# Performance work log

Measured on AMD Instinct MI355X. Metric: run time of the kernel, lower is better.

## Reference

```python
import jax, jax.numpy as jnp
import numpy as np

B, S, QD, DM, H = 8, 4096, 4, 1024, 16
HD = DM // H
NROT = 4
EPS_LN = 1e-5


def layer_norm(x, g, b):
    m = x.mean(axis=-1, keepdims=True)
    v = ((x - m) ** 2).mean(axis=-1, keepdims=True)
    return (x - m) / jnp.sqrt(v + EPS_LN) * g + b


def quat_normalize(q):
    return q / (jnp.linalg.norm(q, axis=-1, keepdims=True) + 1e-8)


def quat_multiply(a, b):
    w1, x1, y1, z1 = a[..., 0], a[..., 1], a[..., 2], a[..., 3]
    w2, x2, y2, z2 = b[..., 0], b[..., 1], b[..., 2], b[..., 3]
    return jnp.stack([
        w1 * w2 - x1 * x2 - y1 * y2 - z1 * z2,
        w1 * x2 + x1 * w2 + y1 * z2 - z1 * y2,
        w1 * y2 - x1 * z2 + y1 * w2 + z1 * x2,
        w1 * z2 + x1 * y2 - y1 * x2 + z1 * w2,
    ], axis=-1)


def quat_conjugate(q):
    return q * jnp.array([1.0, -1.0, -1.0, -1.0], dtype=q.dtype)


def unit_quaternion(theta):  # theta: [3]
    c0, c1, c2 = jnp.cos(theta[0] / 2), jnp.cos(theta[1] / 2), jnp.cos(theta[2] / 2)
    s0, s1, s2 = jnp.sin(theta[0] / 2), jnp.sin(theta[1] / 2), jnp.sin(theta[2] / 2)
    q = jnp.stack([c0 * c1 * c2, s0 * c1 * c2, c0 * s1 * c2, c0 * c1 * s2])
    return quat_normalize(q)


def fractal_alpha(x):  # x: [B, S, DM] -> alpha: [B]
    xf = x.reshape(x.shape[0], -1)
    ps = jnp.abs(jnp.fft.rfft(xf, axis=-1)) ** 2  # [B, N/2+1]
    freqs = jnp.fft.rfftfreq(xf.shape[-1]).astype(x.dtype)
    w = ((freqs > 0.01) & (freqs < 0.5)).astype(x.dtype)
    n = w.sum()
    log_k = jnp.log(freqs + 1e-10)
    log_P = jnp.log(ps + 1e-10)
    mk = (w * log_k).sum() / n
    mP = (w * log_P).sum(axis=-1) / n  # [B]
    dk = (log_k - mk)
    cov = (w * dk * (log_P - mP[:, None])).sum(axis=-1)
    var = (w * dk * dk).sum()
    beta = -cov / (var + 1e-10)
    D = jnp.clip((3.0 - beta) / 2.0, 0.5, 1.5)
    # alpha(D) = alpha_base*(1 + lambda*(D - D_e)/D_e), base=1.0, lambda=0.8, D_e=1.0
    return jnp.clip(1.0 * (1.0 + 0.8 * (D - 1.0)), 0.1, 3.0)


def spectral_attention(x, alpha_base, phase_shift, W_attn_out, b_attn_out, ln_g, ln_b):
    # x: [B, S, DM]
    alpha = jax.lax.stop_gradient(fractal_alpha(x))  # [B]  (torch.no_grad)
    xh = x.reshape(B, S, H, HD).transpose(0, 2, 1, 3)  # [B, H, S, HD]
    x_fft = jnp.fft.fft(xh, axis=2)  # complex [B, H, S, HD]
    freqs = jnp.fft.fftfreq(S).astype(x.dtype)  # [S]
    log_k = jnp.log(jnp.abs(freqs) + 1e-8)
    log_kn = (log_k - log_k.mean()) / (jnp.std(log_k, ddof=1) + 1e-8)
    gelu_k = jax.nn.gelu(log_kn, approximate=False)  # [S]
    # phase[b,h,s] = alpha_base[h]*alpha[b]*gelu_k[s] + phase_shift[h]
    phase = (alpha_base[None, :, None] * alpha[:, None, None] * gelu_k[None, None, :]
             + phase_shift[None, :, None])  # [B, H, S]
    kernel = jnp.exp(1j * phase.astype(jnp.float32))[..., None]  # [B, H, S, 1]
    x_filt = jnp.fft.ifft(x_fft * kernel, axis=2).real  # [B, H, S, HD]
    out = x_filt.transpose(0, 2, 1, 3).reshape(B, S, DM)
    out = out @ W_attn_out + b_attn_out  # out_proj; dropout = identity (eval)
    return layer_norm(x + out, ln_g, ln_b)


def so4_evolution(q, theta_L, theta_R):  # q: [B, S, 4]
    out = q
    for i in range(NROT):
        qL = unit_quaternion(theta_L[i])
        qR_conj = quat_conjugate(unit_quaternion(theta_R[i]))
        out = quat_multiply(quat_multiply(jnp.broadcast_to(qL, out.shape), out),
                            jnp.broadcast_to(qR_conj, out.shape))
        out = quat_normalize(out)
    return out


def setup_inputs() -> dict:
    key = jax.random.key(0)
    ks = jax.random.split(key, 24)
    def rn(k, shape, scale=0.02):
        return jax.random.normal(k, shape, dtype=jnp.float32) * scale
    return {
        "x": jax.random.normal(ks[0], (B, S, QD), dtype=jnp.float32),
        "W_in": rn(ks[1], (QD, DM)), "b_in": jnp.zeros((DM,), jnp.float32),
        "alpha_base": jnp.ones((H,), jnp.float32),
        "phase_shift": jnp.zeros((H,), jnp.float32),
        "W_attn_out": rn(ks[2], (DM, DM)), "b_attn_out": jnp.zeros((DM,), jnp.float32),
        "ln_attn_g": jnp.ones((DM,), jnp.float32), "ln_attn_b": jnp.zeros((DM,), jnp.float32),
        "W_out": rn(ks[3], (DM, QD)), "b_out": jnp.zeros((QD,), jnp.float32),
        "theta_L": rn(ks[4], (NROT, 3), 0.1), "theta_R": rn(ks[5], (NROT, 3), 0.1),
        "W_ff1": rn(ks[6], (QD, 4 * QD)), "b_ff1": jnp.zeros((4 * QD,), jnp.float32),
        "W_ff2": rn(ks[7], (4 * QD, QD)), "b_ff2": jnp.zeros((QD,), jnp.float32),
        "n1_g": jnp.ones((QD,), jnp.float32), "n1_b": jnp.zeros((QD,), jnp.float32),
        "n2_g": jnp.ones((QD,), jnp.float32), "n2_b": jnp.zeros((QD,), jnp.float32),
        "n3_g": jnp.ones((QD,), jnp.float32), "n3_b": jnp.zeros((QD,), jnp.float32),
    }


def reference(x, W_in, b_in, alpha_base, phase_shift, W_attn_out, b_attn_out,
              ln_attn_g, ln_attn_b, W_out, b_out, theta_L, theta_R,
              W_ff1, b_ff1, W_ff2, b_ff2, n1_g, n1_b, n2_g, n2_b, n3_g, n3_b):
    x_proj = x @ W_in + b_in  # [B, S, DM]
    attn = spectral_attention(x_proj, alpha_base, phase_shift, W_attn_out, b_attn_out,
                              ln_attn_g, ln_attn_b)
    attn_quat = attn @ W_out + b_out  # [B, S, 4]
    h = quat_normalize(layer_norm(x + attn_quat, n1_g, n1_b))
    evolved = so4_evolution(h, theta_L, theta_R)
    h = quat_normalize(layer_norm(h + evolved, n2_g, n2_b))
    ff = jax.nn.gelu(h @ W_ff1 + b_ff1, approximate=False) @ W_ff2 + b_ff2
    h = quat_normalize(layer_norm(h + ff, n3_g, n3_b))
    return h
```

## Files before the change

### kernel.cpp

```cpp
#include <hip/hip_runtime.h>
#include <hip/hip_bf16.h>
#include <math.h>


#define DEV static __device__ __forceinline__
typedef unsigned int uint32;
typedef unsigned short u16;

typedef __attribute__((ext_vector_type(8))) _Float16 f16x8;
typedef __attribute__((ext_vector_type(4))) float f32x4;
typedef __attribute__((ext_vector_type(2))) unsigned int u32x2;

DEV float2 cmulf(float2 a, float2 b) {
  return make_float2(a.x * b.x - a.y * b.y, a.x * b.y + a.y * b.x);
}
DEV u16 f2h(float f) {
  union { _Float16 h; u16 u; } v;
  v.h = (_Float16)f;
  return v.u;
}
DEV float h2f(uint32 u) {
  union { u16 s; _Float16 h; } v;
  v.s = (u16)u;
  return (float)v.h;
}
DEV uint32 pack2h(float a, float b) {
  return (uint32)f2h(a) | ((uint32)f2h(b) << 16);
}
DEV void glds16(void* lds, const void* g) {
  __builtin_amdgcn_global_load_lds((const __attribute__((address_space(1))) unsigned int*)g,
                                   (__attribute__((address_space(3))) unsigned int*)lds, 16, 0, 0);
}
DEV void wave_sync() {
  asm volatile("s_waitcnt lgkmcnt(0)" ::: "memory");
  __builtin_amdgcn_sched_barrier(0);
}
DEV int dr10(int v) {
  int r = (int)(__brev((unsigned)v) >> 22);
  return ((r & 0x155) << 1) | ((r & 0x2AA) >> 1);
}
constexpr int dr6c(int v) {
  return ((v & 3) << 4) | (v & 12) | ((v >> 4) & 3);
}

constexpr float CQ[17] = {
  1.0f, 0.995184726672197f, 0.980785280403230f, 0.956940335732209f,
  0.923879532511287f, 0.881921264348355f, 0.831469612302545f, 0.773010453362737f,
  0.707106781186548f, 0.634393284163645f, 0.555570233019602f, 0.471396736825998f,
  0.382683432365090f, 0.290284677254462f, 0.195090322016128f, 0.098017140329561f, 0.0f };
constexpr float twc64(int j) {
  return (j & 63) <= 16 ? CQ[j & 63]
       : (j & 63) <= 32 ? -CQ[32 - (j & 63)]
       : (j & 63) <= 48 ? -CQ[(j & 63) - 32] : CQ[64 - (j & 63)];
}
constexpr float tws64(int j) {
  return (j & 63) <= 16 ? CQ[16 - (j & 63)]
       : (j & 63) <= 32 ? CQ[(j & 63) - 16]
       : (j & 63) <= 48 ? -CQ[48 - (j & 63)] : -CQ[(j & 63) - 48];
}

constexpr float CR_C[16] = {
  1.0f, 0.980785280403230f, 0.923879532511287f, 0.831469612302545f,
  0.707106781186548f, 0.555570233019602f, 0.382683432365090f, 0.195090322016128f,
  0.0f, -0.195090322016128f, -0.382683432365090f, -0.555570233019602f,
  -0.707106781186548f, -0.831469612302545f, -0.923879532511287f, -0.980785280403230f };
constexpr float CR_S[16] = {
  0.0f, 0.195090322016128f, 0.382683432365090f, 0.555570233019602f,
  0.707106781186548f, 0.831469612302545f, 0.923879532511287f, 0.980785280403230f,
  1.0f, 0.980785280403230f, 0.923879532511287f, 0.831469612302545f,
  0.707106781186548f, 0.555570233019602f, 0.382683432365090f, 0.195090322016128f };

template<int SGN>
DEV void rdif64(float2* z) {
  #pragma unroll
  for (int j = 0; j < 16; ++j) {
    float2 x0 = z[j], x1 = z[j + 16], x2 = z[j + 32], x3 = z[j + 48];
    float2 s0 = make_float2(x0.x + x2.x, x0.y + x2.y);
    float2 s1 = make_float2(x0.x - x2.x, x0.y - x2.y);
    float2 s2 = make_float2(x1.x + x3.x, x1.y + x3.y);
    float2 d  = make_float2(x1.x - x3.x, x1.y - x3.y);
    float2 s3 = (SGN < 0) ? make_float2(d.y, -d.x) : make_float2(-d.y, d.x);
    z[j] = make_float2(s0.x + s2.x, s0.y + s2.y);
    const float2 tf1 = make_float2(twc64(j),     (float)SGN * tws64(j));
    const float2 tf2 = make_float2(twc64(2 * j), (float)SGN * tws64(2 * j));
    const float2 tf3 = make_float2(twc64(3 * j), (float)SGN * tws64(3 * j));
    z[j + 16] = cmulf(make_float2(s1.x + s3.x, s1.y + s3.y), tf1);
    z[j + 32] = cmulf(make_float2(s0.x - s2.x, s0.y - s2.y), tf2);
    z[j + 48] = cmulf(make_float2(s1.x - s3.x, s1.y - s3.y), tf3);
  }
  #pragma unroll
  for (int b = 0; b < 64; b += 16)
    #pragma unroll
    for (int j = 0; j < 4; ++j) {
      const int i = b + j;
      float2 x0 = z[i], x1 = z[i + 4], x2 = z[i + 8], x3 = z[i + 12];
      float2 s0 = make_float2(x0.x + x2.x, x0.y + x2.y);
      float2 s1 = make_float2(x0.x - x2.x, x0.y - x2.y);
      float2 s2 = make_float2(x1.x + x3.x, x1.y + x3.y);
      float2 d  = make_float2(x1.x - x3.x, x1.y - x3.y);
      float2 s3 = (SGN < 0) ? make_float2(d.y, -d.x) : make_float2(-d.y, d.x);
      z[i] = make_float2(s0.x + s2.x, s0.y + s2.y);
      const float2 tf1 = make_float2(twc64(4 * j),  (float)SGN * tws64(4 * j));
      const float2 tf2 = make_float2(twc64(8 * j),  (float)SGN * tws64(8 * j));
      const float2 tf3 = make_float2(twc64(12 * j), (float)SGN * tws64(12 * j));
      z[i + 4]  = cmulf(make_float2(s1.x + s3.x, s1.y + s3.y), tf1);
      z[i + 8]  = cmulf(make_float2(s0.x - s2.x, s0.y - s2.y), tf2);
      z[i + 12] = cmulf(make_float2(s1.x - s3.x, s1.y - s3.y), tf3);
    }
  #pragma unroll
  for (int b = 0; b < 64; b += 4) {
    float2 x0 = z[b], x1 = z[b + 1], x2 = z[b + 2], x3 = z[b + 3];
    float2 s0 = make_float2(x0.x + x2.x, x0.y + x2.y);
    float2 s1 = make_float2(x0.x - x2.x, x0.y - x2.y);
    float2 s2 = make_float2(x1.x + x3.x, x1.y + x3.y);
    float2 d  = make_float2(x1.x - x3.x, x1.y - x3.y);
    float2 s3 = (SGN < 0) ? make_float2(d.y, -d.x) : make_float2(-d.y, d.x);
    z[b]     = make_float2(s0.x + s2.x, s0.y + s2.y);
    z[b + 1] = make_float2(s1.x + s3.x, s1.y + s3.y);
    z[b + 2] = make_float2(s0.x - s2.x, s0.y - s2.y);
    z[b + 3] = make_float2(s1.x - s3.x, s1.y - s3.y);
  }
}

template<int SGN>
DEV void rdit64(float2* z) {
  #pragma unroll
  for (int b = 0; b < 64; b += 4) {
    float2 b0 = z[b], b1 = z[b + 1], b2 = z[b + 2], b3 = z[b + 3];
    float2 t0 = make_float2(b0.x + b2.x, b0.y + b2.y);
    float2 t1 = make_float2(b0.x - b2.x, b0.y - b2.y);
    float2 t2 = make_float2(b1.x + b3.x, b1.y + b3.y);
    float2 d  = make_float2(b1.x - b3.x, b1.y - b3.y);
    float2 t3 = (SGN > 0) ? make_float2(-d.y, d.x) : make_float2(d.y, -d.x);
    z[b]     = make_float2(t0.x + t2.x, t0.y + t2.y);
    z[b + 1] = make_float2(t1.x + t3.x, t1.y + t3.y);
    z[b + 2] = make_float2(t0.x - t2.x, t0.y - t2.y);
    z[b + 3] = make_float2(t1.x - t3.x, t1.y - t3.y);
  }
  #pragma unroll
  for (int b = 0; b < 64; b += 16)
    #pragma unroll
    for (int j = 0; j < 4; ++j) {
      const int i = b + j;
      const float2 tf1 = make_float2(twc64(4 * j),  (float)SGN * tws64(4 * j));
      const float2 tf2 = make_float2(twc64(8 * j),  (float)SGN * tws64(8 * j));
      const float2 tf3 = make_float2(twc64(12 * j), (float)SGN * tws64(12 * j));
      float2 b0 = z[i];
      float2 b1 = cmulf(z[i + 4], tf1);
      float2 b2 = cmulf(z[i + 8], tf2);
      float2 b3 = cmulf(z[i + 12], tf3);
      float2 t0 = make_float2(b0.x + b2.x, b0.y + b2.y);
      float2 t1 = make_float2(b0.x - b2.x, b0.y - b2.y);
      float2 t2 = make_float2(b1.x + b3.x, b1.y + b3.y);
      float2 d  = make_float2(b1.x - b3.x, b1.y - b3.y);
      float2 t3 = (SGN > 0) ? make_float2(-d.y, d.x) : make_float2(d.y, -d.x);
      z[i]      = make_float2(t0.x + t2.x, t0.y + t2.y);
      z[i + 4]  = make_float2(t1.x + t3.x, t1.y + t3.y);
      z[i + 8]  = make_float2(t0.x - t2.x, t0.y - t2.y);
      z[i + 12] = make_float2(t1.x - t3.x, t1.y - t3.y);
    }
  #pragma unroll
  for (int j = 0; j < 16; ++j) {
    const float2 tf1 = make_float2(twc64(j),     (float)SGN * tws64(j));
    const float2 tf2 = make_float2(twc64(2 * j), (float)SGN * tws64(2 * j));
    const float2 tf3 = make_float2(twc64(3 * j), (float)SGN * tws64(3 * j));
    float2 b0 = z[j];
    float2 b1 = cmulf(z[j + 16], tf1);
    float2 b2 = cmulf(z[j + 32], tf2);
    float2 b3 = cmulf(z[j + 48], tf3);
    float2 t0 = make_float2(b0.x + b2.x, b0.y + b2.y);
    float2 t1 = make_float2(b0.x - b2.x, b0.y - b2.y);
    float2 t2 = make_float2(b1.x + b3.x, b1.y + b3.y);
    float2 d  = make_float2(b1.x - b3.x, b1.y - b3.y);
    float2 t3 = (SGN > 0) ? make_float2(-d.y, d.x) : make_float2(d.y, -d.x);
    z[j]      = make_float2(t0.x + t2.x, t0.y + t2.y);
    z[j + 16] = make_float2(t1.x + t3.x, t1.y + t3.y);
    z[j + 32] = make_float2(t0.x - t2.x, t0.y - t2.y);
    z[j + 48] = make_float2(t1.x - t3.x, t1.y - t3.y);
  }
}

template<int L, int NLOG, int NSUB, bool WL>
DEV void dif4_stages(float2* F, int lg) {
  #pragma unroll
  for (int st = 0; st < NLOG / 2; ++st) {
    const int qlog = NLOG - 2 - 2 * st;
    const int q = 1 << qlog;
    float bs, bc;
    __sincosf((float)(lg & (q - 1)) * (-1.57079632679489661923f / (float)q), &bs, &bc);
    const float2 base = make_float2(bc, bs);
    #pragma unroll
    for (int u = 0; u < NSUB * (1 << (NLOG - 2)) / L; ++u) {
      const int sub = (u * L) >> (NLOG - 2);
      const int bf = ((u * L) & ((1 << (NLOG - 2)) - 1)) + lg;
      const int jj = ((u * L) % q) * 8 / q;
      const int i1 = (sub << NLOG) + ((bf >> qlog) << (qlog + 2)) + (bf & (q - 1));
      float2 x0 = F[i1], x1 = F[i1 + q], x2 = F[i1 + 2 * q], x3 = F[i1 + 3 * q];
      float2 s0 = make_float2(x0.x + x2.x, x0.y + x2.y);
      float2 s1 = make_float2(x0.x - x2.x, x0.y - x2.y);
      float2 s2 = make_float2(x1.x + x3.x, x1.y + x3.y);
      float2 dq = make_float2(x1.x - x3.x, x1.y - x3.y);
      float2 s3 = make_float2(dq.y, -dq.x);
      F[i1] = make_float2(s0.x + s2.x, s0.y + s2.y);
      if (qlog == 0) {
        F[i1 + 1] = make_float2(s1.x + s3.x, s1.y + s3.y);
        F[i1 + 2] = make_float2(s0.x - s2.x, s0.y - s2.y);
        F[i1 + 3] = make_float2(s1.x - s3.x, s1.y - s3.y);
      } else {
        const float2 tf1 = (jj == 0) ? base : cmulf(base, make_float2(CR_C[jj], -CR_S[jj]));
        const float2 tf2 = cmulf(tf1, tf1);
        const float2 tf3 = cmulf(tf2, tf1);
        F[i1 + q]     = cmulf(make_float2(s1.x + s3.x, s1.y + s3.y), tf1);
        F[i1 + 2 * q] = cmulf(make_float2(s0.x - s2.x, s0.y - s2.y), tf2);
        F[i1 + 3 * q] = cmulf(make_float2(s1.x - s3.x, s1.y - s3.y), tf3);
      }
    }
    if (WL) wave_sync(); else __syncthreads();
  }
}

DEV float4 qmul4(float4 a, float4 b) {
  return make_float4(
    a.x * b.x - a.y * b.y - a.z * b.z - a.w * b.w,
    a.x * b.y + a.y * b.x + a.z * b.w - a.w * b.z,
    a.x * b.z - a.y * b.w + a.z * b.x + a.w * b.y,
    a.x * b.w + a.y * b.z - a.z * b.y + a.w * b.x);
}
DEV float4 qne(float4 q) {
  float n = sqrtf(q.x * q.x + q.y * q.y + q.z * q.z + q.w * q.w) + 1e-8f;
  float r = 1.0f / n;
  return make_float4(q.x * r, q.y * r, q.z * r, q.w * r);
}

__global__ __launch_bounds__(512) void kx_fr_pass1(const float* __restrict__ x,
    const float* __restrict__ W_in, const float* __restrict__ b_in,
    float2* __restrict__ zmid) {
  __shared__ float2 fb[8 * 1028];
  const int t = threadIdx.x, l = t & 63, w = t >> 6;
  const int btile = blockIdx.x, bz = blockIdx.y;
  const int bcol = btile * 8 + w;
  const int d = 2 * (bcol & 511);
  const int soff = bcol >> 9;
  const float w00 = W_in[d],     w10 = W_in[1024 + d], w20 = W_in[2048 + d], w30 = W_in[3072 + d];
  const float w01 = W_in[d + 1], w11 = W_in[1025 + d], w21 = W_in[2049 + d], w31 = W_in[3073 + d];
  const float bi0 = b_in[d], bi1 = b_in[d + 1];
  const float* xb = x + (size_t)bz * 4096 * 4;
  float2* fbw = fb + w * 1028;
  #pragma unroll
  for (int i = 0; i < 16; ++i) {
    int a = i * 64 + l;
    int s = 4 * a + soff;
    float4 xv = *(const float4*)(xb + (size_t)s * 4);
    float z0 = fmaf(xv.x, w00, fmaf(xv.y, w10, fmaf(xv.z, w20, fmaf(xv.w, w30, bi0))));
    float z1 = fmaf(xv.x, w01, fmaf(xv.y, w11, fmaf(xv.z, w21, fmaf(xv.w, w31, bi1))));
    fbw[a] = make_float2(z0, z1);
  }
  wave_sync();
  dif4_stages<64, 10, 1, true>(fbw, l);
  __syncthreads();
  float2* dst = zmid + (size_t)bz * (1024 * 2048);
  #pragma unroll
  for (int i = 0; i < 16; ++i) {
    int idx = i * 512 + t;
    int w8 = idx & 7, cnat = idx >> 3;
    float2 v = fb[w8 * 1028 + dr10(cnat)];
    dst[(size_t)cnat * 2048 + btile * 8 + w8] = v;
  }
}

DEV float block_reduce128(float* red, int t, float v) {
  red[t] = v; __syncthreads();
  for (int s = 64; s; s >>= 1) { if (t < s) red[t] += red[t + s]; __syncthreads(); }
  float r = red[0]; __syncthreads();
  return r;
}

__global__ __launch_bounds__(128) void kx_fr_pass2(const float2* __restrict__ zmid,
    float* __restrict__ partials, float* __restrict__ sparts) {
  __shared__ float2 fb[2 * 2052];
  __shared__ float red[128];
  const int t = threadIdx.x, l = t & 63, w = t >> 6;
  const int cg = blockIdx.x, bz = blockIdx.y;
  const int c = (cg == 0) ? (w ? 512 : 0) : (w ? (1024 - cg) : cg);
  const float2* src = zmid + ((size_t)bz * 1024 + c) * 2048;
  float2* fbc = fb + w * 2052;
  float2 rot[4], stp4;
  {
    float sn, cs;
    __sincosf((float)(l * c) * (-6.28318530717958647692f / 2097152.0f), &sn, &cs);
    rot[0] = make_float2(cs, sn);
    float2 stp;
    __sincosf((float)c * (-6.28318530717958647692f / 32768.0f), &sn, &cs);
    stp = make_float2(cs, sn);
    rot[1] = cmulf(rot[0], stp);
    float2 stp2 = cmulf(stp, stp);
    rot[2] = cmulf(rot[0], stp2);
    rot[3] = cmulf(rot[1], stp2);
    stp4 = cmulf(stp2, stp2);
  }
  float2 zr[32];
  #pragma unroll
  for (int i = 0; i < 32; ++i) {
    int bb = i * 64 + l;
    zr[i] = cmulf(src[bb], rot[i & 3]);
    rot[i & 3] = cmulf(rot[i & 3], stp4);
  }
  {
    float bs, bc;
    __sincosf((float)l * (-3.14159265358979323846f / 1024.0f), &bs, &bc);
    const float2 b2 = make_float2(bc, bs);
    #pragma unroll
    for (int u = 0; u < 16; ++u) {
      const float2 tf = (u == 0) ? b2 : cmulf(b2, make_float2(CR_C[u], -CR_S[u]));
      int i1 = u * 64 + l;
      float2 a0 = zr[u], a1 = zr[u + 16];
      fbc[i1] = make_float2(a0.x + a1.x, a0.y + a1.y);
      fbc[i1 + 1024] = cmulf(make_float2(a0.x - a1.x, a0.y - a1.y), tf);
    }
    wave_sync();
  }
  dif4_stages<64, 10, 2, true>(fbc, l);
  __syncthreads();
  float t0 = 0.f, t1 = 0.f, s0 = 0.f, s1 = 0.f, s2 = 0.f;
  if (cg != 0) {
    const float2* fbm = fb + (1 - w) * 2052;
    float2 pw[32];
    pw[0] = make_float2(1.f, 0.f);
    {
      float sn, cs;
      __sincosf(-3.14159265358979323846f / 2048.0f, &sn, &cs);
      float2 w1 = make_float2(cs, sn);
      #pragma unroll
      for (int j = 1; j < 32; ++j) pw[j] = cmulf(pw[j - 1], w1);
    }
    const int drl = (l & 3) * 256 + ((l >> 2) & 3) * 64 + ((l >> 4) & 3) * 16;
    float2 base2;
    {
      float sn, cs;
      __sincosf((float)drl * (-3.14159265358979323846f / 1024.0f), &sn, &cs);
      float2 lf = make_float2(cs, sn);
      __sincosf((float)c * (-6.28318530717958647692f / 4194304.0f), &sn, &cs);
      base2 = cmulf(make_float2(cs, sn), lf);
    }
    #pragma unroll
    for (int i = 0; i < 32; ++i) {
      const int p = i * 64 + l;
      const int dri = (i & 3) * 4 + ((i >> 2) & 3);
      const int top = i >> 4;
      const int dd = 2 * (drl + dri) + top;
      float2 Zk = fbc[p];
      float2 Zm = fbm[2047 - p];
      float2 E = make_float2(0.5f * (Zk.x + Zm.x), 0.5f * (Zk.y - Zm.y));
      float2 A = make_float2(Zk.x - Zm.x, Zk.y + Zm.y);
      float2 O = make_float2(0.5f * A.y, -0.5f * A.x);
      float2 urot = cmulf(base2, pw[2 * dri + top]);
      float2 U = cmulf(urot, O);
      float Xr = E.x + U.x, Xi = E.y + U.y;
      float P = Xr * Xr + Xi * Xi;
      int k = c + (dd << 10);
      float fr = (float)k * (1.0f / 4194304.0f);
      if (fr > 0.01f && fr < 0.5f) {
        float lp = __logf(P + 1e-10f);
        float lk = __logf(fr + 1e-10f);
        t0 += lp; t1 += lk * lp;
        s0 += 1.0f; s1 += lk; s2 += lk * lk;
      }
    }
  } else {
    const float2* fbm = fbc;
    float2 urot;
    {
      float sn, cs;
      __sincosf((float)(c + l * 1024) * (-6.28318530717958647692f / 4194304.0f), &sn, &cs);
      urot = make_float2(cs, sn);
    }
    const float2 ustp = make_float2(0.995184726672197f, -0.0980171403295606f);
    #pragma unroll
    for (int i = 0; i < 32; ++i) {
      int dd = i * 64 + l;
      int md = (c == 0) ? ((2048 - dd) & 2047) : (2047 - dd);
      int pk = ((dd & 1) << 10) | dr10(dd >> 1);
      int pm = ((md & 1) << 10) | dr10(md >> 1);
      float2 Zk = fbc[pk];
      float2 Zm = fbm[pm];
      float2 E = make_float2(0.5f * (Zk.x + Zm.x), 0.5f * (Zk.y - Zm.y));
      float2 A = make_float2(Zk.x - Zm.x, Zk.y + Zm.y);
      float2 O = make_float2(0.5f * A.y, -0.5f * A.x);
      float2 U = cmulf(urot, O);
      float Xr = E.x + U.x, Xi = E.y + U.y;
      float P = Xr * Xr + Xi * Xi;
      int k = c + (dd << 10);
      float fr = (float)k * (1.0f / 4194304.0f);
      if (fr > 0.01f && fr < 0.5f) {
        float lp = __logf(P + 1e-10f);
        float lk = __logf(fr + 1e-10f);
        t0 += lp; t1 += lk * lp;
        s0 += 1.0f; s1 += lk; s2 += lk * lk;
      }
      urot = cmulf(urot, ustp);
    }
  }
  float T0 = block_reduce128(red, t, t0);
  float T1 = block_reduce128(red, t, t1);
  if (t == 0) {
    partials[((size_t)bz * 512 + cg) * 2 + 0] = T0;
    partials[((size_t)bz * 512 + cg) * 2 + 1] = T1;
  }
  if (bz == 0) {
    float S0 = block_reduce128(red, t, s0);
    float S1 = block_reduce128(red, t, s1);
    float S2 = block_reduce128(red, t, s2);
    if (t == 0) { sparts[cg * 3] = S0; sparts[cg * 3 + 1] = S1; sparts[cg * 3 + 2] = S2; }
  }
}

DEV float block_reduce512(float* sh, int t, float v) {
  sh[t] = v; __syncthreads();
  for (int s = 256; s; s >>= 1) { if (t < s) sh[t] += sh[t + s]; __syncthreads(); }
  float r = sh[0]; __syncthreads();
  return r;
}

__global__ __launch_bounds__(512) void kx_finalize(const float* __restrict__ partials,
    const float* __restrict__ sparts, float* __restrict__ alpha, float* __restrict__ gelu) {
  __shared__ float sh[512];
  __shared__ float lk[4096];
  const int t = threadIdx.x;
  float S0 = block_reduce512(sh, t, sparts[t * 3 + 0]);
  float S1 = block_reduce512(sh, t, sparts[t * 3 + 1]);
  float S2 = block_reduce512(sh, t, sparts[t * 3 + 2]);
  float mk = S1 / S0;
  float var = S2 - mk * S1;
  for (int b = 0; b < 8; ++b) {
    float T0 = block_reduce512(sh, t, partials[((size_t)b * 512 + t) * 2 + 0]);
    float T1 = block_reduce512(sh, t, partials[((size_t)b * 512 + t) * 2 + 1]);
    if (t == 0) {
      float cov = T1 - mk * T0;
      float beta = -cov / (var + 1e-10f);
      float D = fminf(fmaxf((3.0f - beta) * 0.5f, 0.5f), 1.5f);
      alpha[b] = fminf(fmaxf(1.0f + 0.8f * (D - 1.0f), 0.1f), 3.0f);
    }
  }
  for (int s = t; s < 4096; s += 512) {
    int m = (s < 2048) ? s : (4096 - s);
    lk[s] = logf((float)m * (1.0f / 4096.0f) + 1e-8f);
  }
  __syncthreads();
  float ls = 0.f;
  for (int s = t; s < 4096; s += 512) ls += lk[s];
  float mean = block_reduce512(sh, t, ls) * (1.0f / 4096.0f);
  float vs = 0.f;
  for (int s = t; s < 4096; s += 512) { float dv = lk[s] - mean; vs += dv * dv; }
  float sd = sqrtf(block_reduce512(sh, t, vs) * (1.0f / 4095.0f));
  for (int k = t; k < 2049; k += 512) {
    float xn = (lk[k] - mean) / (sd + 1e-8f);
    gelu[k] = 0.5f * xn * (1.0f + erff(xn * 0.70710678118654752440f));
  }
}

__global__ __launch_bounds__(256) void kx_gains(const float* __restrict__ alpha,
    const float* __restrict__ gelu, const float* __restrict__ abase,
    const float* __restrict__ pshift, const float* __restrict__ thL,
    const float* __restrict__ thR, float* __restrict__ gains, float* __restrict__ qlr) {
  const int bh = blockIdx.x;
  const float aa = abase[bh & 15] * alpha[bh >> 4];
  const float ps = pshift[bh & 15];
  for (int k = threadIdx.x; k < 2049; k += 256)
    gains[(size_t)bh * 2064 + k] = cosf(fmaf(aa, gelu[k], ps));
  if (bh == 0 && threadIdx.x == 0) {
    float4 QL = make_float4(1.f, 0.f, 0.f, 0.f);
    float4 QRC = make_float4(1.f, 0.f, 0.f, 0.f);
    for (int it = 0; it < 4; ++it) {
      float s0, c0, s1, c1, s2, c2;
      sincosf(0.5f * thL[it * 3 + 0], &s0, &c0);
      sincosf(0.5f * thL[it * 3 + 1], &s1, &c1);
      sincosf(0.5f * thL[it * 3 + 2], &s2, &c2);
      float4 qL = qne(make_float4(c0 * c1 * c2, s0 * c1 * c2, c0 * s1 * c2, c0 * c1 * s2));
      QL = qmul4(qL, QL);
      sincosf(0.5f * thR[it * 3 + 0], &s0, &c0);
      sincosf(0.5f * thR[it * 3 + 1], &s1, &c1);
      sincosf(0.5f * thR[it * 3 + 2], &s2, &c2);
      float4 qR = qne(make_float4(c0 * c1 * c2, s0 * c1 * c2, c0 * s1 * c2, c0 * c1 * s2));
      QRC = qmul4(QRC, make_float4(qR.x, -qR.y, -qR.z, -qR.w));
    }
    *(float4*)qlr = QL;
    *(float4*)(qlr + 4) = QRC;
  }
}

__global__ __launch_bounds__(256) void kx_wt(const float* __restrict__ W, u16* __restrict__ Wt) {
  __shared__ float tile[64][65];
  const int t = threadIdx.x;
  const int nt = blockIdx.x, dt = blockIdx.y;
  #pragma unroll
  for (int i = 0; i < 16; ++i) {
    int idx = i * 256 + t;
    int r = idx >> 6, cc = idx & 63;
    tile[r][cc] = W[(size_t)(dt * 64 + r) * 1024 + nt * 64 + cc];
  }
  __syncthreads();
  #pragma unroll
  for (int i = 0; i < 2; ++i) {
    int task = i * 256 + t;
    int nl = task >> 3, g = task & 7;
    union { u16 h[8]; uint4 v; } pk;
    #pragma unroll
    for (int k = 0; k < 8; ++k) pk.h[k] = f2h(tile[g * 8 + k][nl]);
    size_t idx = (size_t)(nt * 64 + nl) * 1024 + dt * 64 + ((g ^ (nl & 7)) << 3);
    *(uint4*)(Wt + idx) = pk.v;
  }
}

__global__ __launch_bounds__(128, 1) void kx_filter(const float* __restrict__ x,
    const float* __restrict__ W_in, const float* __restrict__ b_in,
    const float* __restrict__ gains, uint32* __restrict__ XFp) {
  __shared__ uint32 tr[2][4096];
  const int t = threadIdx.x, l = t & 63, wv = t >> 6;
  const int g = blockIdx.x, h = blockIdx.y, bz = blockIdx.z;
  const int d0 = h * 64 + g * 4 + wv * 2;
  const float* gn = gains + ((size_t)bz * 16 + h) * 2064;
  const float wa0 = W_in[d0],     wa1 = W_in[1024 + d0], wa2 = W_in[2048 + d0], wa3 = W_in[3072 + d0];
  const float wb0 = W_in[d0 + 1], wb1 = W_in[1025 + d0], wb2 = W_in[2049 + d0], wb3 = W_in[3073 + d0];
  const float bia = b_in[d0], bib = b_in[d0 + 1];
  const float* xb = x + (size_t)bz * 4096 * 4;
  uint32* trw = tr[wv];
  float2 z[64];
  #pragma unroll
  for (int r = 0; r < 64; ++r) {
    int s = r * 64 + l;
    float4 xv = *(const float4*)(xb + (size_t)s * 4);
    float za = fmaf(xv.x, wa0, fmaf(xv.y, wa1, fmaf(xv.z, wa2, fmaf(xv.w, wa3, bia))));
    float zb = fmaf(xv.x, wb0, fmaf(xv.y, wb1, fmaf(xv.z, wb2, fmaf(xv.w, wb3, bib))));
    z[r] = make_float2(za, zb);
  }
  rdif64<-1>(z);
  {
    float sn, cs;
    __sincosf((float)l * (-6.28318530717958647692f / 4096.0f), &sn, &cs);
    float2 w1 = make_float2(cs, sn);
    float2 w2 = cmulf(w1, w1);
    float2 w4 = cmulf(w2, w2);
    float2 tch[4] = { make_float2(1.f, 0.f), w1, w2, cmulf(w2, w1) };
    #pragma unroll
    for (int i = 0; i < 16; ++i) {
      #pragma unroll
      for (int j = 0; j < 4; ++j) {
        const int rr = dr6c(4 * i + j);
        z[rr] = cmulf(z[rr], tch[j]);
      }
      #pragma unroll
      for (int j = 0; j < 4; ++j) tch[j] = cmulf(tch[j], w4);
    }
  }
  #pragma unroll
  for (int r = 0; r < 64; ++r) {
    const int k1 = dr6c(r);
    trw[k1 * 64 + ((l + k1) & 63)] = pack2h(z[r].x, z[r].y);
  }
  wave_sync();
  #pragma unroll
  for (int c = 0; c < 64; ++c) {
    uint32 u = trw[l * 64 + ((c + l) & 63)];
    z[c] = make_float2(h2f(u & 0xFFFFu), h2f(u >> 16));
  }
  wave_sync();
  rdif64<-1>(z);
  #pragma unroll
  for (int r = 0; r < 64; ++r) {
    const int k = l + (dr6c(r) << 6);
    const int km = (k < 2048) ? k : (4096 - k);
    const float gk = gn[km];
    z[r] = make_float2(z[r].x * gk, z[r].y * gk);
  }
  rdit64<1>(z);
  {
    float sn, cs;
    __sincosf((float)l * (6.28318530717958647692f / 4096.0f), &sn, &cs);
    float2 v1 = make_float2(cs, sn);
    float2 v2 = cmulf(v1, v1);
    float2 v4 = cmulf(v2, v2);
    float2 tch[4] = { make_float2(1.f, 0.f), v1, v2, cmulf(v2, v1) };
    #pragma unroll
    for (int i = 0; i < 16; ++i) {
      #pragma unroll
      for (int j = 0; j < 4; ++j)
        z[4 * i + j] = cmulf(z[4 * i + j], tch[j]);
      #pragma unroll
      for (int j = 0; j < 4; ++j) tch[j] = cmulf(tch[j], v4);
    }
  }
  #pragma unroll
  for (int r = 0; r < 64; ++r)
    trw[r * 64 + ((l + r) & 63)] = pack2h(z[r].x, z[r].y);
  wave_sync();
  #pragma unroll
  for (int c = 0; c < 64; ++c) {
    uint32 u = trw[l * 64 + ((c + l) & 63)];
    z[c] = make_float2(h2f(u & 0xFFFFu), h2f(u >> 16));
  }
  wave_sync();
  #pragma unroll
  for (int j = 0; j < 64; ++j) {
    const int dj = dr6c(j);
    if (dj > j) { float2 tmp = z[j]; z[j] = z[dj]; z[dj] = tmp; }
  }
  rdit64<1>(z);
  uint32* rowp = XFp + ((size_t)bz * 512 + (d0 >> 1)) * 4096;
  const float sc = 1.0f / 4096.0f;
  #pragma unroll
  for (int r = 0; r < 64; ++r)
    rowp[r * 64 + l] = pack2h(z[r].x * sc, z[r].y * sc);
}

__global__ __launch_bounds__(256) void kx_a16(const uint32* __restrict__ XFp, uint32* __restrict__ Aswz) {
  __shared__ uint32 tl[64][65];
  const int t = threadIdx.x;
  const int st = blockIdx.x, pt = blockIdx.y, bz = blockIdx.z;
  const uint32* src = XFp + ((size_t)bz * 512 + pt * 64) * 4096 + st * 64;
  #pragma unroll
  for (int i = 0; i < 16; ++i) {
    int p = i * 4 + (t >> 6);
    int s = t & 63;
    tl[p][s] = src[(size_t)p * 4096 + s];
  }
  __syncthreads();
  uint32* dst = Aswz + ((size_t)bz * 4096 + st * 64) * 512 + pt * 64;
  #pragma unroll
  for (int i = 0; i < 16; ++i) {
    int s = i * 4 + (t >> 6);
    int c = t & 63;
    int gsl = ((c & 31) >> 2) ^ (s & 7);
    int u32idx = (c >> 5) * 32 + gsl * 4 + (c & 3);
    dst[(size_t)s * 512 + u32idx] = tl[c][s];
  }
}

__global__ __launch_bounds__(256) void kx_gemm(const u16* __restrict__ A,
    const u16* __restrict__ Bw, u16* __restrict__ C) {
  __shared__ u16 sm[32768];
  const int t = threadIdx.x, l = t & 63, w = t >> 6;
  const int wm = w >> 1, wn = w & 1;
  const int id = blockIdx.x;
  const int wg = (id & 7) * 256 + (id >> 3);
  const int bm = wg >> 3, bn = wg & 7;
  const int bh = bm >> 5;
  const u16* Ab = A + ((size_t)(bh * 4096 + (bm & 31) * 128)) * 1024;
  const u16* Bb = Bw + (size_t)(bn * 128) * 1024;
  const int fr = l & 15;
  const int lr = l >> 3, lg = l & 7;
  f32x4 acc[4][4];
  #pragma unroll
  for (int m = 0; m < 4; ++m)
    #pragma unroll
    for (int n = 0; n < 4; ++n) acc[m][n] = (f32x4){0.f, 0.f, 0.f, 0.f};

  #define STAGE(KT, BUF) { \
    u16* Ad = sm + (BUF) * 8192; \
    u16* Bd = sm + 16384 + (BUF) * 8192; \
    _Pragma("unroll") \
    for (int j = 0; j < 4; ++j) { \
      int qq = j * 4 + w; \
      glds16((void*)(Ad + qq * 512), Ab + (size_t)(qq * 8 + lr) * 1024 + (KT) * 64 + lg * 8); \
      glds16((void*)(Bd + qq * 512), Bb + (size_t)(qq * 8 + lr) * 1024 + (KT) * 64 + lg * 8); \
    } }

  STAGE(0, 0);
  __syncthreads();
  for (int kt = 0; kt < 16; ++kt) {
    const int cur = kt & 1;
    if (kt < 15) STAGE(kt + 1, cur ^ 1);
    const u16* Ac = sm + cur * 8192;
    const u16* Bc = sm + 16384 + cur * 8192;
    #pragma unroll
    for (int kk = 0; kk < 2; ++kk) {
      const int g8r = kk * 4 + (l >> 4);
      f16x8 af[4], bf[4];
      #pragma unroll
      for (int m = 0; m < 4; ++m) {
        int s = wm * 64 + m * 16 + fr;
        af[m] = *(const f16x8*)&Ac[s * 64 + ((g8r ^ (s & 7)) << 3)];
      }
      #pragma unroll
      for (int n = 0; n < 4; ++n) {
        int nn = wn * 64 + n * 16 + fr;
        bf[n] = *(const f16x8*)&Bc[nn * 64 + ((g8r ^ (nn & 7)) << 3)];
      }
      #pragma unroll
      for (int m = 0; m < 4; ++m)
        #pragma unroll
        for (int n = 0; n < 4; ++n)
          acc[m][n] = __builtin_amdgcn_mfma_f32_16x16x32_f16(af[m], bf[n], acc[m][n], 0, 0, 0);
    }
    __syncthreads();
  }
  float* Cs = (float*)sm;
  const int rl4 = (l >> 4) * 4;
  #pragma unroll
  for (int m = 0; m < 4; ++m) {
    int rbase = wm * 64 + m * 16 + rl4;
    #pragma unroll
    for (int n = 0; n < 4; ++n) {
      int cc = wn * 64 + n * 16 + fr;
      #pragma unroll
      for (int e = 0; e < 4; ++e) {
        int r = rbase + e;
        Cs[r * 128 + (cc ^ (((r >> 2) & 3) << 3))] = acc[m][n][e];
      }
    }
  }
  __syncthreads();
  u16* cgp = C + (size_t)(bm * 128) * 1024 + bn * 128;
  #pragma unroll
  for (int it = 0; it < 16; ++it) {
    int idx = it * 256 + t;
    int r = idx >> 5, c4 = (idx & 31) * 4;
    f32x4 v = *(const f32x4*)&Cs[r * 128 + (c4 ^ (((r >> 2) & 3) << 3))];
    u32x2 pv;
    pv.x = (uint32)f2h(v.x) | ((uint32)f2h(v.y) << 16);
    pv.y = (uint32)f2h(v.z) | ((uint32)f2h(v.w) << 16);
    __builtin_nontemporal_store(pv, (u32x2*)(cgp + (size_t)r * 1024 + c4));
  }
}

DEV float wred64(float v) {
  #pragma unroll
  for (int m = 32; m; m >>= 1) v += __shfl_xor(v, m);
  return v;
}
DEV float4 ln4q(float4 v, const float* g, const float* b) {
  float m = 0.25f * (v.x + v.y + v.z + v.w);
  float a0 = v.x - m, a1 = v.y - m, a2 = v.z - m, a3 = v.w - m;
  float var = 0.25f * (a0 * a0 + a1 * a1 + a2 * a2 + a3 * a3);
  float rs = 1.0f / sqrtf(var + 1e-5f);
  return make_float4(a0 * rs * g[0] + b[0], a1 * rs * g[1] + b[1],
                     a2 * rs * g[2] + b[2], a3 * rs * g[3] + b[3]);
}
DEV float gelu1(float v) { return 0.5f * v * (1.0f + erff(v * 0.70710678118654752440f)); }

__global__ __launch_bounds__(256) void kx_tail(const u16* __restrict__ G,
    const float* __restrict__ x, const float* __restrict__ W_in, const float* __restrict__ b_in,
    const float* __restrict__ b_attn, const float* __restrict__ lng, const float* __restrict__ lnb,
    const float* __restrict__ W_out, const float* __restrict__ b_out,
    const float* __restrict__ qlr,
    const float* __restrict__ Wf1, const float* __restrict__ bff1,
    const float* __restrict__ Wf2, const float* __restrict__ bff2,
    const float* __restrict__ n1g, const float* __restrict__ n1b,
    const float* __restrict__ n2g, const float* __restrict__ n2b,
    const float* __restrict__ n3g, const float* __restrict__ n3b,
    float* __restrict__ out) {
  const int l = threadIdx.x & 63, w = threadIdx.x >> 6;
  const size_t rg = (size_t)blockIdx.x * 4 + w;
  const float4 x4 = *(const float4*)(x + rg * 4);
  float4 tv[4];
  float lsum = 0.f;
  #pragma unroll
  for (int j = 0; j < 4; ++j) {
    int dd = j * 256 + l * 4;
    uint2 gv = *(const uint2*)(G + rg * 1024 + dd);
    float4 g4 = make_float4(h2f(gv.x & 0xFFFFu), h2f(gv.x >> 16),
                            h2f(gv.y & 0xFFFFu), h2f(gv.y >> 16));
    float4 w0 = *(const float4*)(W_in + dd);
    float4 w1 = *(const float4*)(W_in + 1024 + dd);
    float4 w2 = *(const float4*)(W_in + 2048 + dd);
    float4 w3 = *(const float4*)(W_in + 3072 + dd);
    float4 bi = *(const float4*)(b_in + dd);
    float4 ba = *(const float4*)(b_attn + dd);
    float4 o;
    o.x = g4.x + bi.x + ba.x + x4.x * w0.x + x4.y * w1.x + x4.z * w2.x + x4.w * w3.x;
    o.y = g4.y + bi.y + ba.y + x4.x * w0.y + x4.y * w1.y + x4.z * w2.y + x4.w * w3.y;
    o.z = g4.z + bi.z + ba.z + x4.x * w0.z + x4.y * w1.z + x4.z * w2.z + x4.w * w3.z;
    o.w = g4.w + bi.w + ba.w + x4.x * w0.w + x4.y * w1.w + x4.z * w2.w + x4.w * w3.w;
    tv[j] = o;
    lsum += o.x + o.y + o.z + o.w;
  }
  const float mean = wred64(lsum) * (1.0f / 1024.0f);
  float vsum = 0.f;
  #pragma unroll
  for (int j = 0; j < 4; ++j) {
    float a0 = tv[j].x - mean, a1 = tv[j].y - mean, a2 = tv[j].z - mean, a3 = tv[j].w - mean;
    vsum += a0 * a0 + a1 * a1 + a2 * a2 + a3 * a3;
  }
  const float rstd = 1.0f / sqrtf(wred64(vsum) * (1.0f / 1024.0f) + 1e-5f);
  float4 aq = make_float4(0.f, 0.f, 0.f, 0.f);
  #pragma unroll
  for (int j = 0; j < 4; ++j) {
    int dd = j * 256 + l * 4;
    float4 gg = *(const float4*)(lng + dd);
    float4 bb = *(const float4*)(lnb + dd);
    float av[4];
    av[0] = (tv[j].x - mean) * rstd * gg.x + bb.x;
    av[1] = (tv[j].y - mean) * rstd * gg.y + bb.y;
    av[2] = (tv[j].z - mean) * rstd * gg.z + bb.z;
    av[3] = (tv[j].w - mean) * rstd * gg.w + bb.w;
    #pragma unroll
    for (int e = 0; e < 4; ++e) {
      float4 wr = *(const float4*)(W_out + (size_t)(dd + e) * 4);
      aq.x = fmaf(av[e], wr.x, aq.x);
      aq.y = fmaf(av[e], wr.y, aq.y);
      aq.z = fmaf(av[e], wr.z, aq.z);
      aq.w = fmaf(av[e], wr.w, aq.w);
    }
  }
  aq.x = wred64(aq.x) + b_out[0];
  aq.y = wred64(aq.y) + b_out[1];
  aq.z = wred64(aq.z) + b_out[2];
  aq.w = wred64(aq.w) + b_out[3];
  float4 q1 = make_float4(x4.x + aq.x, x4.y + aq.y, x4.z + aq.z, x4.w + aq.w);
  float4 hq = qne(ln4q(q1, n1g, n1b));
  const float4 QL = *(const float4*)qlr;
  const float4 QRC = *(const float4*)(qlr + 4);
  float4 o = qne(qmul4(qmul4(QL, hq), QRC));
  float4 h2 = qne(ln4q(make_float4(hq.x + o.x, hq.y + o.y, hq.z + o.z, hq.w + o.w), n2g, n2b));
  float ffx = 0.f, ffy = 0.f, ffz = 0.f, ffw = 0.f;
  if (l < 16) {
    float uv = bff1[l] + h2.x * Wf1[l] + h2.y * Wf1[16 + l] + h2.z * Wf1[32 + l] + h2.w * Wf1[48 + l];
    uv = gelu1(uv);
    float4 w2r = *(const float4*)(Wf2 + l * 4);
    ffx = uv * w2r.x; ffy = uv * w2r.y; ffz = uv * w2r.z; ffw = uv * w2r.w;
  }
  ffx = wred64(ffx) + bff2[0];
  ffy = wred64(ffy) + bff2[1];
  ffz = wred64(ffz) + bff2[2];
  ffw = wred64(ffw) + bff2[3];
  float4 h3 = qne(ln4q(make_float4(h2.x + ffx, h2.y + ffy, h2.z + ffz, h2.w + ffw), n3g, n3b));
  if (l == 0) *(float4*)(out + rg * 4) = h3;
}

extern "C" void kernel_launch(void* const* d_in, const int* in_sizes, int n_in,
                              void* d_out, int out_size, void* d_ws, size_t ws_size,
                              hipStream_t stream) {
  (void)in_sizes; (void)n_in; (void)out_size;
  const float* x      = (const float*)d_in[0];
  const float* W_in   = (const float*)d_in[1];
  const float* b_in   = (const float*)d_in[2];
  const float* abase  = (const float*)d_in[3];
  const float* pshift = (const float*)d_in[4];
  const float* Wattn  = (const float*)d_in[5];
  const float* battn  = (const float*)d_in[6];
  const float* lng    = (const float*)d_in[7];
  const float* lnb    = (const float*)d_in[8];
  const float* Wout   = (const float*)d_in[9];
  const float* bout   = (const float*)d_in[10];
  const float* thL    = (const float*)d_in[11];
  const float* thR    = (const float*)d_in[12];
  const float* Wf1    = (const float*)d_in[13];
  const float* bff1   = (const float*)d_in[14];
  const float* Wf2    = (const float*)d_in[15];
  const float* bff2   = (const float*)d_in[16];
  const float* n1g    = (const float*)d_in[17];
  const float* n1b    = (const float*)d_in[18];
  const float* n2g    = (const float*)d_in[19];
  const float* n2b    = (const float*)d_in[20];
  const float* n3g    = (const float*)d_in[21];
  const float* n3b    = (const float*)d_in[22];

  if (ws_size < (size_t)138459204) return;
  char* ws = (char*)d_ws;
  float2* Zmid  = (float2*)ws;
  uint32* XFp   = (uint32*)ws;
  u16*   Aswz   = (u16*)(ws + 67108864);
  u16*   C16    = (u16*)ws;
  u16*   W2h    = (u16*)(ws + 134217728);
  float* gainsw = (float*)(ws + 136314880);
  float* qlrw   = (float*)(ws + 137400320);
  float* partials = (float*)(ws + 138412032);
  float* sparts   = (float*)(ws + 138444800);
  float* alphaw   = (float*)(ws + 138450944);
  float* geluw    = (float*)(ws + 138451008);

  kx_fr_pass1<<<dim3(256, 8), 512, 0, stream>>>(x, W_in, b_in, Zmid);
  kx_fr_pass2<<<dim3(512, 8), 128, 0, stream>>>(Zmid, partials, sparts);
  kx_finalize<<<1, 512, 0, stream>>>(partials, sparts, alphaw, geluw);
  kx_gains<<<128, 256, 0, stream>>>(alphaw, geluw, abase, pshift, thL, thR, gainsw, qlrw);
  kx_wt<<<dim3(16, 16), 256, 0, stream>>>(Wattn, W2h);
  kx_filter<<<dim3(16, 16, 8), 128, 0, stream>>>(x, W_in, b_in, gainsw, XFp);
  kx_a16<<<dim3(64, 8, 8), 256, 0, stream>>>(XFp, (uint32*)Aswz);
  kx_gemm<<<2048, 256, 0, stream>>>(Aswz, W2h, C16);
  kx_tail<<<8192, 256, 0, stream>>>(C16, x, W_in, b_in, battn, lng, lnb, Wout, bout,
                                    qlrw, Wf1, bff1, Wf2, bff2,
                                    n1g, n1b, n2g, n2b, n3g, n3b, (float*)d_out);
}
```

Baseline: 440.2 us.

## Store intermediate FFT in fp16 and merge gain/finalize/weight-transpose kernels

The pass1 row-FFT output is packed as fp16 pairs, halving the global traffic of the large intermediate buffer read by pass2. The finalize, gains and weight-transpose kernels are fused into one launch, with each gains block redundantly recomputing the alpha statistics and log-frequency GELU values. This removes two launches and a single-block serial kernel. It trades away precision in the spectral power estimate used for alpha, and the pass2 shared-memory padding is dropped.

```diff
diff --git a/kernel.cpp b/kernel.cpp
--- a/kernel.cpp
+++ b/kernel.cpp
@@ -26,6 +26,9 @@
 }
 DEV uint32 pack2h(float a, float b) {
   return (uint32)f2h(a) | ((uint32)f2h(b) << 16);
+}
+DEV float2 unp2h(uint32 u) {
+  return make_float2(h2f(u & 0xFFFFu), h2f(u >> 16));
 }
 DEV void glds16(void* lds, const void* g) {
   __builtin_amdgcn_global_load_lds((const __attribute__((address_space(1))) unsigned int*)g,
@@ -234,7 +237,7 @@
 
 __global__ __launch_bounds__(512) void kx_fr_pass1(const float* __restrict__ x,
     const float* __restrict__ W_in, const float* __restrict__ b_in,
-    float2* __restrict__ zmid) {
+    uint32* __restrict__ zmid) {
   __shared__ float2 fb[8 * 1028];
   const int t = threadIdx.x, l = t & 63, w = t >> 6;
   const int btile = blockIdx.x, bz = blockIdx.y;
@@ -258,13 +261,13 @@
   wave_sync();
   dif4_stages<64, 10, 1, true>(fbw, l);
   __syncthreads();
-  float2* dst = zmid + (size_t)bz * (1024 * 2048);
+  uint32* dst = zmid + (size_t)bz * (1024 * 2048);
   #pragma unroll
   for (int i = 0; i < 16; ++i) {
     int idx = i * 512 + t;
     int w8 = idx & 7, cnat = idx >> 3;
     float2 v = fb[w8 * 1028 + dr10(cnat)];
-    dst[(size_t)cnat * 2048 + btile * 8 + w8] = v;
+    dst[(size_t)cnat * 2048 + btile * 8 + w8] = pack2h(v.x, v.y);
   }
 }
 
@@ -275,15 +278,14 @@
   return r;
 }
 
-__global__ __launch_bounds__(128) void kx_fr_pass2(const float2* __restrict__ zmid,
+__global__ __launch_bounds__(128) void kx_fr_pass2(const uint32* __restrict__ zmid,
     float* __restrict__ partials, float* __restrict__ sparts) {
-  __shared__ float2 fb[2 * 2052];
-  __shared__ float red[128];
+  __shared__ float2 fb[2 * 2048];
   const int t = threadIdx.x, l = t & 63, w = t >> 6;
   const int cg = blockIdx.x, bz = blockIdx.y;
   const int c = (cg == 0) ? (w ? 512 : 0) : (w ? (1024 - cg) : cg);
-  const float2* src = zmid + ((size_t)bz * 1024 + c) * 2048;
-  float2* fbc = fb + w * 2052;
+  const uint32* src = zmid + ((size_t)bz * 1024 + c) * 2048;
+  float2* fbc = fb + w * 2048;
   float2 rot[4], stp4;
   {
     float sn, cs;
@@ -302,7 +304,7 @@
   #pragma unroll
   for (int i = 0; i < 32; ++i) {
     int bb = i * 64 + l;
-    zr[i] = cmulf(src[bb], rot[i & 3]);
+    zr[i] = cmulf(unp2h(src[bb]), rot[i & 3]);
     rot[i & 3] = cmulf(rot[i & 3], stp4);
   }
   {
@@ -323,7 +325,7 @@
   __syncthreads();
   float t0 = 0.f, t1 = 0.f, s0 = 0.f, s1 = 0.f, s2 = 0.f;
   if (cg != 0) {
-    const float2* fbm = fb + (1 - w) * 2052;
+    const float2* fbm = fb + (1 - w) * 2048;
     float2 pw[32];
     pw[0] = make_float2(1.f, 0.f);
     {
@@ -400,6 +402,8 @@
       urot = cmulf(urot, ustp);
     }
   }
+  __syncthreads();
+  float* red = (float*)fb;
   float T0 = block_reduce128(red, t, t0);
   float T1 = block_reduce128(red, t, t1);
   if (t == 0) {
@@ -414,100 +418,105 @@
   }
 }
 
-DEV float block_reduce512(float* sh, int t, float v) {
+DEV float block_reduce256s(float* sh, int t, float v) {
   sh[t] = v; __syncthreads();
-  for (int s = 256; s; s >>= 1) { if (t < s) sh[t] += sh[t + s]; __syncthreads(); }
+  for (int s = 128; s; s >>= 1) { if (t < s) sh[t] += sh[t + s]; __syncthreads(); }
   float r = sh[0]; __syncthreads();
   return r;
 }
 
-__global__ __launch_bounds__(512) void kx_finalize(const float* __restrict__ partials,
-    const float* __restrict__ sparts, float* __restrict__ alpha, float* __restrict__ gelu) {
-  __shared__ float sh[512];
-  __shared__ float lk[4096];
+__global__ __launch_bounds__(256) void kx_gainsall(const float* __restrict__ partials,
+    const float* __restrict__ sparts, const float* __restrict__ abase,
+    const float* __restrict__ pshift, const float* __restrict__ thL,
+    const float* __restrict__ thR, const float* __restrict__ W,
+    u16* __restrict__ Wt, float* __restrict__ gains, float* __restrict__ qlr) {
+  const int bid = blockIdx.x;
   const int t = threadIdx.x;
-  float S0 = block_reduce512(sh, t, sparts[t * 3 + 0]);
-  float S1 = block_reduce512(sh, t, sparts[t * 3 + 1]);
-  float S2 = block_reduce512(sh, t, sparts[t * 3 + 2]);
-  float mk = S1 / S0;
-  float var = S2 - mk * S1;
-  for (int b = 0; b < 8; ++b) {
-    float T0 = block_reduce512(sh, t, partials[((size_t)b * 512 + t) * 2 + 0]);
-    float T1 = block_reduce512(sh, t, partials[((size_t)b * 512 + t) * 2 + 1]);
-    if (t == 0) {
-      float cov = T1 - mk * T0;
-      float beta = -cov / (var + 1e-10f);
-      float D = fminf(fmaxf((3.0f - beta) * 0.5f, 0.5f), 1.5f);
-      alpha[b] = fminf(fmaxf(1.0f + 0.8f * (D - 1.0f), 0.1f), 3.0f);
-    }
-  }
-  for (int s = t; s < 4096; s += 512) {
+  if (bid >= 128) {
+    __shared__ float tile[64][65];
+    const int q = bid - 128;
+    const int nt = q & 15, dt = q >> 4;
+    #pragma unroll
+    for (int i = 0; i < 16; ++i) {
+      int idx = i * 256 + t;
+      int r = idx >> 6, cc = idx & 63;
+      tile[r][cc] = W[(size_t)(dt * 64 + r) * 1024 + nt * 64 + cc];
+    }
+    __syncthreads();
+    #pragma unroll
+    for (int i = 0; i < 2; ++i) {
+      int task = i * 256 + t;
+      int nl = task >> 3, g = task & 7;
+      union { u16 h[8]; uint4 v; } pk;
+      #pragma unroll
+      for (int k = 0; k < 8; ++k) pk.h[k] = f2h(tile[g * 8 + k][nl]);
+      size_t idx = (size_t)(nt * 64 + nl) * 1024 + dt * 64 + ((g ^ (nl & 7)) << 3);
+      *(uint4*)(Wt + idx) = pk.v;
+    }
+    return;
+  }
+  __shared__ float red[256];
+  float s0 = 0.f, s1 = 0.f, s2 = 0.f;
+  for (int i = t; i < 512; i += 256) {
+    s0 += sparts[i * 3]; s1 += sparts[i * 3 + 1]; s2 += sparts[i * 3 + 2];
+  }
+  s0 = block_reduce256s(red, t, s0);
+  s1 = block_reduce256s(red, t, s1);
+  s2 = block_reduce256s(red, t, s2);
+  const float mk = s1 / s0;
+  const float var = s2 - mk * s1;
+  const int b = bid >> 4, h = bid & 15;
+  float t0 = 0.f, t1 = 0.f;
+  for (int i = t; i < 512; i += 256) {
+    t0 += partials[((size_t)b * 512 + i) * 2];
+    t1 += partials[((size_t)b * 512 + i) * 2 + 1];
+  }
+  t0 = block_reduce256s(red, t, t0);
+  t1 = block_reduce256s(red, t, t1);
+  const float cov = t1 - mk * t0;
+  const float beta = -cov / (var + 1e-10f);
+  const float D = fminf(fmaxf((3.0f - beta) * 0.5f, 0.5f), 1.5f);
+  const float alpha = fminf(fmaxf(1.0f + 0.8f * (D - 1.0f), 0.1f), 3.0f);
+  const float aa = abase[h] * alpha;
+  const float ps = pshift[h];
+  float lkv[16];
+  float ls = 0.f;
+  #pragma unroll
+  for (int i = 0; i < 16; ++i) {
+    int s = i * 256 + t;
     int m = (s < 2048) ? s : (4096 - s);
-    lk[s] = logf((float)m * (1.0f / 4096.0f) + 1e-8f);
-  }
-  __syncthreads();
-  float ls = 0.f;
-  for (int s = t; s < 4096; s += 512) ls += lk[s];
-  float mean = block_reduce512(sh, t, ls) * (1.0f / 4096.0f);
+    lkv[i] = logf((float)m * (1.0f / 4096.0f) + 1e-8f);
+    ls += lkv[i];
+  }
+  const float mean = block_reduce256s(red, t, ls) * (1.0f / 4096.0f);
   float vs = 0.f;
-  for (int s = t; s < 4096; s += 512) { float dv = lk[s] - mean; vs += dv * dv; }
-  float sd = sqrtf(block_reduce512(sh, t, vs) * (1.0f / 4095.0f));
-  for (int k = t; k < 2049; k += 512) {
-    float xn = (lk[k] - mean) / (sd + 1e-8f);
-    gelu[k] = 0.5f * xn * (1.0f + erff(xn * 0.70710678118654752440f));
-  }
-}
-
-__global__ __launch_bounds__(256) void kx_gains(const float* __restrict__ alpha,
-    const float* __restrict__ gelu, const float* __restrict__ abase,
-    const float* __restrict__ pshift, const float* __restrict__ thL,
-    const float* __restrict__ thR, float* __restrict__ gains, float* __restrict__ qlr) {
-  const int bh = blockIdx.x;
-  const float aa = abase[bh & 15] * alpha[bh >> 4];
-  const float ps = pshift[bh & 15];
-  for (int k = threadIdx.x; k < 2049; k += 256)
-    gains[(size_t)bh * 2064 + k] = cosf(fmaf(aa, gelu[k], ps));
-  if (bh == 0 && threadIdx.x == 0) {
+  #pragma unroll
+  for (int i = 0; i < 16; ++i) { float dv = lkv[i] - mean; vs += dv * dv; }
+  const float sd = sqrtf(block_reduce256s(red, t, vs) * (1.0f / 4095.0f));
+  for (int k = t; k < 2049; k += 256) {
+    float lk_k = logf((float)k * (1.0f / 4096.0f) + 1e-8f);
+    float xn = (lk_k - mean) / (sd + 1e-8f);
+    float ge = 0.5f * xn * (1.0f + erff(xn * 0.70710678118654752440f));
+    gains[(size_t)bid * 2064 + k] = cosf(fmaf(aa, ge, ps));
+  }
+  if (bid == 0 && t == 0) {
     float4 QL = make_float4(1.f, 0.f, 0.f, 0.f);
     float4 QRC = make_float4(1.f, 0.f, 0.f, 0.f);
     for (int it = 0; it < 4; ++it) {
-      float s0, c0, s1, c1, s2, c2;
-      sincosf(0.5f * thL[it * 3 + 0], &s0, &c0);
-      sincosf(0.5f * thL[it * 3 + 1], &s1, &c1);
-      sincosf(0.5f * thL[it * 3 + 2], &s2, &c2);
-      float4 qL = qne(make_float4(c0 * c1 * c2, s0 * c1 * c2, c0 * s1 * c2, c0 * c1 * s2));
+      float ss0, cc0, ss1, cc1, ss2, cc2;
+      sincosf(0.5f * thL[it * 3 + 0], &ss0, &cc0);
+      sincosf(0.5f * thL[it * 3 + 1], &ss1, &cc1);
+      sincosf(0.5f * thL[it * 3 + 2], &ss2, &cc2);
+      float4 qL = qne(make_float4(cc0 * cc1 * cc2, ss0 * cc1 * cc2, cc0 * ss1 * cc2, cc0 * cc1 * ss2));
       QL = qmul4(qL, QL);
-      sincosf(0.5f * thR[it * 3 + 0], &s0, &c0);
-      sincosf(0.5f * thR[it * 3 + 1], &s1, &c1);
-      sincosf(0.5f * thR[it * 3 + 2], &s2, &c2);
-      float4 qR = qne(make_float4(c0 * c1 * c2, s0 * c1 * c2, c0 * s1 * c2, c0 * c1 * s2));
+      sincosf(0.5f * thR[it * 3 + 0], &ss0, &cc0);
+      sincosf(0.5f * thR[it * 3 + 1], &ss1, &cc1);
+      sincosf(0.5f * thR[it * 3 + 2], &ss2, &cc2);
+      float4 qR = qne(make_float4(cc0 * cc1 * cc2, ss0 * cc1 * cc2, cc0 * ss1 * cc2, cc0 * cc1 * ss2));
       QRC = qmul4(QRC, make_float4(qR.x, -qR.y, -qR.z, -qR.w));
     }
     *(float4*)qlr = QL;
     *(float4*)(qlr + 4) = QRC;
-  }
-}
-
-__global__ __launch_bounds__(256) void kx_wt(const float* __restrict__ W, u16* __restrict__ Wt) {
-  __shared__ float tile[64][65];
-  const int t = threadIdx.x;
-  const int nt = blockIdx.x, dt = blockIdx.y;
-  #pragma unroll
-  for (int i = 0; i < 16; ++i) {
-    int idx = i * 256 + t;
-    int r = idx >> 6, cc = idx & 63;
-    tile[r][cc] = W[(size_t)(dt * 64 + r) * 1024 + nt * 64 + cc];
-  }
-  __syncthreads();
-  #pragma unroll
-  for (int i = 0; i < 2; ++i) {
-    int task = i * 256 + t;
-    int nl = task >> 3, g = task & 7;
-    union { u16 h[8]; uint4 v; } pk;
-    #pragma unroll
-    for (int k = 0; k < 8; ++k) pk.h[k] = f2h(tile[g * 8 + k][nl]);
-    size_t idx = (size_t)(nt * 64 + nl) * 1024 + dt * 64 + ((g ^ (nl & 7)) << 3);
-    *(uint4*)(Wt + idx) = pk.v;
   }
 }
 
@@ -561,7 +570,7 @@
   #pragma unroll
   for (int c = 0; c < 64; ++c) {
     uint32 u = trw[l * 64 + ((c + l) & 63)];
-    z[c] = make_float2(h2f(u & 0xFFFFu), h2f(u >> 16));
+    z[c] = unp2h(u);
   }
   wave_sync();
   rdif64<-1>(z);
@@ -596,7 +605,7 @@
   #pragma unroll
   for (int c = 0; c < 64; ++c) {
     uint32 u = trw[l * 64 + ((c + l) & 63)];
-    z[c] = make_float2(h2f(u & 0xFFFFu), h2f(u >> 16));
+    z[c] = unp2h(u);
   }
   wave_sync();
   #pragma unroll
@@ -856,7 +865,7 @@
 
   if (ws_size < (size_t)138459204) return;
   char* ws = (char*)d_ws;
-  float2* Zmid  = (float2*)ws;
+  uint32* Zmid  = (uint32*)ws;
   uint32* XFp   = (uint32*)ws;
   u16*   Aswz   = (u16*)(ws + 67108864);
   u16*   C16    = (u16*)ws;
@@ -865,14 +874,11 @@
   float* qlrw   = (float*)(ws + 137400320);
   float* partials = (float*)(ws + 138412032);
   float* sparts   = (float*)(ws + 138444800);
-  float* alphaw   = (float*)(ws + 138450944);
-  float* geluw    = (float*)(ws + 138451008);
 
   kx_fr_pass1<<<dim3(256, 8), 512, 0, stream>>>(x, W_in, b_in, Zmid);
   kx_fr_pass2<<<dim3(512, 8), 128, 0, stream>>>(Zmid, partials, sparts);
-  kx_finalize<<<1, 512, 0, stream>>>(partials, sparts, alphaw, geluw);
-  kx_gains<<<128, 256, 0, stream>>>(alphaw, geluw, abase, pshift, thL, thR, gainsw, qlrw);
-  kx_wt<<<dim3(16, 16), 256, 0, stream>>>(Wattn, W2h);
+  kx_gainsall<<<384, 256, 0, stream>>>(partials, sparts, abase, pshift, thL, thR,
+                                       Wattn, W2h, gainsw, qlrw);
   kx_filter<<<dim3(16, 16, 8), 128, 0, stream>>>(x, W_in, b_in, gainsw, XFp);
   kx_a16<<<dim3(64, 8, 8), 256, 0, stream>>>(XFp, (uint32*)Aswz);
   kx_gemm<<<2048, 256, 0, stream>>>(Aswz, W2h, C16);
```

After: 417.9 us. 5.1% less time.
